# Performance work log

Measured on AMD Instinct MI355X. Metric: run time of the kernel, lower is better.

## Reference

```python
import jax, jax.numpy as jnp
import numpy as np

N_NODES = 50000
N_GRAPHS = 128


def gcn_conv(x, W, b, src, dst, n_nodes):
    """PyG-style GCNConv: add self-loops, symmetric normalization, linear transform, scatter-add."""
    # linear transform first (PyG applies lin before propagate)
    h = x @ W  # [N, out]
    loop = jnp.arange(n_nodes, dtype=src.dtype)
    src_f = jnp.concatenate([src, loop])  # [E+N]
    dst_f = jnp.concatenate([dst, loop])
    # degree over destination (incl. self-loops), edge weight = 1
    deg = jax.ops.segment_sum(jnp.ones_like(src_f, dtype=h.dtype), dst_f, num_segments=n_nodes)
    dinv = jnp.where(deg > 0, jax.lax.rsqrt(deg), 0.0)
    norm = dinv[src_f] * dinv[dst_f]  # [E+N]
    msg = h[src_f] * norm[:, None]  # gather + scale
    out = jax.ops.segment_sum(msg, dst_f, num_segments=n_nodes)  # scatter-add
    return out + b


def setup_inputs() -> dict:
    key = jax.random.key(0)
    k = jax.random.split(key, 8)
    in_c, hid_c, out_c = 128, 128, 64
    x = jax.random.normal(k[0], (N_NODES, in_c), dtype=jnp.float32)
    edge_index = jax.random.randint(k[1], (2, 625000), 0, N_NODES, dtype=jnp.int64)
    batch = jnp.sort(jax.random.randint(k[2], (N_NODES,), 0, N_GRAPHS, dtype=jnp.int64))
    # Glorot-style init for GCN weights, zero bias (PyG default)
    W1 = jax.random.normal(k[3], (in_c, hid_c), dtype=jnp.float32) / np.sqrt(in_c)
    b1 = jnp.zeros((hid_c,), dtype=jnp.float32)
    W2 = jax.random.normal(k[4], (hid_c, out_c), dtype=jnp.float32) / np.sqrt(hid_c)
    b2 = jnp.zeros((out_c,), dtype=jnp.float32)
    return {"x": x, "W1": W1, "b1": b1, "W2": W2, "b2": b2,
            "edge_index": edge_index, "batch": batch}


def reference(x, W1, b1, W2, b2, edge_index, batch):
    src, dst = edge_index[0], edge_index[1]
    h = gcn_conv(x, W1, b1, src, dst, N_NODES)
    h = jax.nn.relu(h)
    h = gcn_conv(h, W2, b2, src, dst, N_NODES)  # [N, out_c]
    # global_mean_pool: segment mean over batch vector
    sums = jax.ops.segment_sum(h, batch, num_segments=N_GRAPHS)  # [G, out_c]
    counts = jax.ops.segment_sum(jnp.ones((h.shape[0],), dtype=h.dtype), batch, num_segments=N_GRAPHS)
    return sums / jnp.maximum(counts, 1.0)[:, None]
```

## Files before the change

kernel.cpp:

```cpp
#include <hip/hip_runtime.h>
#include <hip/hip_bf16.h>
#include <hip/hip_fp8.h>
#include <stdint.h>

typedef __hip_bfloat16  bf16;
typedef __hip_bfloat162 bf2;

typedef __attribute__((ext_vector_type(8))) short short8v;
typedef __attribute__((ext_vector_type(4))) float float4v;

#define KSLOT 48
#define CSTRIDE 16

static __device__ __forceinline__ uint32_t pack2(float a, float b) {
  bf2 t = __float22bfloat162_rn(make_float2(a, b));
  return *(uint32_t*)&t;
}
static __device__ __forceinline__ float fp8_to_f(unsigned char b) {
  __hip_fp8_e4m3 t; t.__x = (__hip_fp8_storage_t)b; return (float)t;
}
static __device__ __forceinline__ unsigned char f_to_fp8(float f) {
  __hip_fp8_e4m3 t(f); return (unsigned char)t.__x;
}

union U16x8 { uint32_t u[4]; uint4 q; short8v v; };

#define NB_FILL 306
#define NB_GEMM 782


__global__ void k_prep(const float* __restrict__ W1, const float* __restrict__ W2,
                       ushort* __restrict__ Ws1, ushort* __restrict__ Ws2,
                       const int* __restrict__ batch, int* __restrict__ gstart,
                       int n, int G) {
  const int tid = threadIdx.x;
  if (blockIdx.x == 0) {
    for (int idx = tid; idx < 2048; idx += 256) {
      int t = idx >> 8, c = (idx >> 6) & 3, l = idx & 63;
      int kbase = c * 32 + (l >> 4) * 8, colg = t * 16 + (l & 15);
      U16x8 u;
#pragma unroll
      for (int j = 0; j < 4; ++j)
        u.u[j] = pack2(W1[(size_t)(kbase + 2 * j) * 128 + colg],
                       W1[(size_t)(kbase + 2 * j + 1) * 128 + colg]);
      *(uint4*)&Ws1[(size_t)idx * 8] = u.q;
    }
  } else {
    for (int idx = tid; idx < 1024; idx += 256) {
      int t = idx >> 8, c = (idx >> 6) & 3, l = idx & 63;
      int kbase = c * 32 + (l >> 4) * 8, colg = t * 16 + (l & 15);
      U16x8 u;
#pragma unroll
      for (int j = 0; j < 4; ++j)
        u.u[j] = pack2(W2[(size_t)(kbase + 2 * j) * 64 + colg],
                       W2[(size_t)(kbase + 2 * j + 1) * 64 + colg]);
      *(uint4*)&Ws2[(size_t)idx * 8] = u.q;
    }
    if (tid <= G) {
      int lo = 0, hi = n;
      while (lo < hi) {
        int mid = (lo + hi) >> 1;
        if (batch[mid] < tid) lo = mid + 1; else hi = mid;
      }
      gstart[tid] = lo;
    }
  }
}


__global__ __launch_bounds__(256) void k_fused(
    const float* __restrict__ A, const ushort* __restrict__ Ws1,
    unsigned char* __restrict__ C, int n,
    const int* __restrict__ src, const int* __restrict__ dst,
    int* __restrict__ cntS, ushort* __restrict__ slots, int E) {
  __shared__ ushort Wf[2048 * 8];
  const int bid = blockIdx.x;
  const int tid = threadIdx.x;

  if (bid < NB_FILL) {
    int base = bid * 2048 + tid;
#pragma unroll
    for (int j = 0; j < 8; ++j) {
      int e = base + j * 256;
      if (e < E) {
        int d = dst[e];
        int p = atomicAdd(&cntS[d << 4], 1);
        if (p < KSLOT) slots[(size_t)d * KSLOT + p] = (ushort)src[e];
      }
    }
  } else {
    for (int idx = tid; idx < 2048; idx += 256)
      *(uint4*)&Wf[(size_t)idx * 8] = *(const uint4*)&Ws1[(size_t)idx * 8];
    __syncthreads();
    const int row0 = (bid - NB_FILL) * 64;
    const int w = tid >> 6, lane = tid & 63;
    const int m = lane & 15, q = lane >> 4;
    const int gr = row0 + w * 16 + m;
    float4v acc[8];
#pragma unroll
    for (int t = 0; t < 8; ++t) acc[t] = (float4v){0.f, 0.f, 0.f, 0.f};
    for (int c = 0; c < 4; ++c) {
      U16x8 a;
      if (gr < n) {
        const float* ap = &A[(size_t)gr * 128 + c * 32 + q * 8];
        float4 f0 = *(const float4*)ap;
        float4 f1 = *(const float4*)(ap + 4);
        a.u[0] = pack2(f0.x, f0.y); a.u[1] = pack2(f0.z, f0.w);
        a.u[2] = pack2(f1.x, f1.y); a.u[3] = pack2(f1.z, f1.w);
      } else {
        a.q = make_uint4(0, 0, 0, 0);
      }
#pragma unroll
      for (int t = 0; t < 8; ++t) {
        U16x8 b;
        b.q = *(const uint4*)&Wf[((size_t)(t * 4 + c) * 64 + lane) * 8];
        acc[t] = __builtin_amdgcn_mfma_f32_16x16x32_bf16(a.v, b.v, acc[t], 0, 0, 0);
      }
    }
#pragma unroll
    for (int reg = 0; reg < 4; ++reg) {
      int gor = row0 + w * 16 + q * 4 + reg;
      if (gor < n) {
#pragma unroll
        for (int t = 0; t < 8; ++t)
          C[(size_t)gor * 128 + t * 16 + m] = f_to_fp8(acc[t][reg]);
      }
    }
  }
}

__global__ void k_dinv(const int* __restrict__ cntS, float* __restrict__ dinv, int n) {
  int i = blockIdx.x * blockDim.x + threadIdx.x;
  if (i < n) dinv[i] = rsqrtf((float)(cntS[i << 4] + 1));
}


__global__ __launch_bounds__(256) void k_gemm64(const bf16* __restrict__ A,
                                                const ushort* __restrict__ Ws2,
                                                unsigned char* __restrict__ C, int n) {
  __shared__ ushort Wf[1024 * 8];
  const int tid = threadIdx.x;
  const int row0 = blockIdx.x * 64;
  for (int idx = tid; idx < 1024; idx += 256)
    *(uint4*)&Wf[(size_t)idx * 8] = *(const uint4*)&Ws2[(size_t)idx * 8];
  __syncthreads();
  const int w = tid >> 6, lane = tid & 63;
  const int m = lane & 15, q = lane >> 4;
  const int gr = row0 + w * 16 + m;
  float4v acc[4];
#pragma unroll
  for (int t = 0; t < 4; ++t) acc[t] = (float4v){0.f, 0.f, 0.f, 0.f};
  for (int c = 0; c < 4; ++c) {
    U16x8 a;
    if (gr < n) {
      a.q = *(const uint4*)&A[(size_t)gr * 128 + c * 32 + q * 8];
    } else {
      a.q = make_uint4(0, 0, 0, 0);
    }
#pragma unroll
    for (int t = 0; t < 4; ++t) {
      U16x8 b;
      b.q = *(const uint4*)&Wf[((size_t)(t * 4 + c) * 64 + lane) * 8];
      acc[t] = __builtin_amdgcn_mfma_f32_16x16x32_bf16(a.v, b.v, acc[t], 0, 0, 0);
    }
  }
#pragma unroll
  for (int reg = 0; reg < 4; ++reg) {
    int gor = row0 + w * 16 + q * 4 + reg;
    if (gor < n) {
#pragma unroll
      for (int t = 0; t < 4; ++t)
        C[(size_t)gor * 64 + t * 16 + m] = f_to_fp8(acc[t][reg]);
    }
  }
}


__global__ void k_agg1(const unsigned char* __restrict__ h, const float* __restrict__ dinv,
                       const int* __restrict__ cntS, const ushort* __restrict__ slots,
                       const float* __restrict__ b1, bf16* __restrict__ out, int n) {
  int wid = threadIdx.x >> 6, lane = threadIdx.x & 63;
  int v = blockIdx.x * 4 + wid;
  if (v >= n) return;
  float dv = dinv[v];
  ushort sraw = ((const ushort*)(h + (size_t)v * 128))[lane];
  float ax = fp8_to_f((unsigned char)(sraw & 0xff)) * dv;
  float ay = fp8_to_f((unsigned char)(sraw >> 8)) * dv;
  int deg = min(cntS[v << 4], KSLOT);
  const ushort* sl = slots + (size_t)v * KSLOT;
  for (int e = 0; e < deg; e += 8) {
    uint4 u8 = *(const uint4*)&sl[e];
    int id[8] = {(int)(u8.x & 0xffff), (int)(u8.x >> 16), (int)(u8.y & 0xffff), (int)(u8.y >> 16),
                 (int)(u8.z & 0xffff), (int)(u8.z >> 16), (int)(u8.w & 0xffff), (int)(u8.w >> 16)};
    float w[8];
#pragma unroll
    for (int j = 0; j < 8; ++j) {
      bool live = (e + j < deg);
      id[j] = live ? id[j] : v;
      w[j] = live ? dinv[id[j]] : 0.f;
    }
    ushort raw[8];
#pragma unroll
    for (int j = 0; j < 8; ++j)
      raw[j] = ((const ushort*)(h + (size_t)id[j] * 128))[lane];
#pragma unroll
    for (int j = 0; j < 8; ++j) {
      ax += w[j] * fp8_to_f((unsigned char)(raw[j] & 0xff));
      ay += w[j] * fp8_to_f((unsigned char)(raw[j] >> 8));
    }
  }
  float2 bb = ((const float2*)b1)[lane];
  float rx = fmaxf(ax * dv + bb.x, 0.f);
  float ry = fmaxf(ay * dv + bb.y, 0.f);
  ((bf2*)(out + (size_t)v * 128))[lane] = __float22bfloat162_rn(make_float2(rx, ry));
}

__global__ void k_agg2(const unsigned char* __restrict__ h, const float* __restrict__ dinv,
                       const int* __restrict__ cntS, const ushort* __restrict__ slots,
                       const float* __restrict__ b2, float* __restrict__ o2, int n) {
  int wid = threadIdx.x >> 6, lane = threadIdx.x & 63;
  int v = blockIdx.x * 4 + wid;
  if (v >= n) return;
  float dv = dinv[v];
  float acc = fp8_to_f(h[(size_t)v * 64 + lane]) * dv;
  int deg = min(cntS[v << 4], KSLOT);
  const ushort* sl = slots + (size_t)v * KSLOT;
  for (int e = 0; e < deg; e += 8) {
    uint4 u8 = *(const uint4*)&sl[e];
    int id[8] = {(int)(u8.x & 0xffff), (int)(u8.x >> 16), (int)(u8.y & 0xffff), (int)(u8.y >> 16),
                 (int)(u8.z & 0xffff), (int)(u8.z >> 16), (int)(u8.w & 0xffff), (int)(u8.w >> 16)};
    float w[8];
#pragma unroll
    for (int j = 0; j < 8; ++j) {
      bool live = (e + j < deg);
      id[j] = live ? id[j] : v;
      w[j] = live ? dinv[id[j]] : 0.f;
    }
    unsigned char raw[8];
#pragma unroll
    for (int j = 0; j < 8; ++j)
      raw[j] = h[(size_t)id[j] * 64 + lane];
#pragma unroll
    for (int j = 0; j < 8; ++j) acc += w[j] * fp8_to_f(raw[j]);
  }
  o2[(size_t)v * 64 + lane] = acc * dv + b2[lane];
}

__global__ void k_pool(const float* __restrict__ o2, const int* __restrict__ gstart,
                       float* __restrict__ out) {
  int g = blockIdx.x;
  int s = gstart[g], epos = gstart[g + 1];
  int lane = threadIdx.x & 63, wid = threadIdx.x >> 6;
  float acc = 0.f;
  for (int i = s + wid; i < epos; i += 4)
    acc += o2[(size_t)i * 64 + lane];
  __shared__ float red[4][64];
  red[wid][lane] = acc;
  __syncthreads();
  if (wid == 0) {
    float v = red[0][lane] + red[1][lane] + red[2][lane] + red[3][lane];
    float c = (float)max(epos - s, 1);
    out[g * 64 + lane] = v / c;
  }
}


extern "C" void kernel_launch(void* const* d_in, const int* in_sizes, int n_in,
                              void* d_out, int out_size, void* d_ws, size_t ws_size,
                              hipStream_t stream) {
  const float* x   = (const float*)d_in[0];
  const float* W1  = (const float*)d_in[1];
  const float* b1  = (const float*)d_in[2];
  const float* W2  = (const float*)d_in[3];
  const float* b2  = (const float*)d_in[4];
  const int* ei    = (const int*)d_in[5];
  const int* batch = (const int*)d_in[6];

  const int n = in_sizes[0] / 128;
  const int E = in_sizes[5] / 2;
  const int G = 128;

  const int* src = ei;
  const int* dst = ei + E;

  char* ws = (char*)d_ws;
  size_t off = 0;
  auto alloc = [&](size_t bytes) -> void* {
    void* p = ws + off;
    off = (off + bytes + 255) & ~(size_t)255;
    return p;
  };
  unsigned char* h1 = (unsigned char*)alloc((size_t)n * 128);
  bf16*   a1    = (bf16*)alloc((size_t)n * 128 * 2);
  ushort* slots = (ushort*)alloc((size_t)n * KSLOT * 2);
  int*    cntS  = (int*)alloc((size_t)n * CSTRIDE * 4);
  float*  dinv  = (float*)alloc((size_t)n * 4);
  int*    gstart= (int*)alloc((size_t)(G + 1) * 4);
  ushort* Ws1   = (ushort*)alloc(2048 * 16);
  ushort* Ws2   = (ushort*)alloc(1024 * 16);
  unsigned char* h2 = h1;
  float*  o2 = (float*)a1;
  float*  out = (float*)d_out;

  hipMemsetAsync(cntS, 0, (size_t)n * CSTRIDE * 4, stream);

  k_prep<<<2, 256, 0, stream>>>(W1, W2, Ws1, Ws2, batch, gstart, n, G);
  k_fused<<<NB_FILL + NB_GEMM, 256, 0, stream>>>(x, Ws1, h1, n, src, dst, cntS, slots, E);
  k_dinv<<<(n + 255) / 256, 256, 0, stream>>>(cntS, dinv, n);
  k_agg1<<<(n + 3) / 4, 256, 0, stream>>>(h1, dinv, cntS, slots, b1, a1, n);
  k_gemm64<<<(n + 63) / 64, 256, 0, stream>>>(a1, Ws2, h2, n);
  k_agg2<<<(n + 3) / 4, 256, 0, stream>>>(h2, dinv, cntS, slots, b2, o2, n);
  k_pool<<<G, 256, 0, stream>>>(o2, gstart, out);
}
```

Before: 206.4 us.

## Fuse layer-1 aggregation with second GEMM and pooling into aggregation via atomics

Merges the layer-1 aggregation, ReLU and the 128x64 MFMA GEMM into one kernel that keeps each 16-node tile of activations in shared memory, so the bf16 intermediate never goes to global memory. It also folds mean pooling into the layer-2 aggregation through atomicAdd scaled by a precomputed inverse graph size, with the output pre-seeded with the bias. Finally, the cntS memset moves into extra blocks of the prep kernel. This removes two kernel launches, a memset and intermediate global traffic. In exchange it adds atomic contention on the 128x64 output and gives lower occupancy in the fused kernel. The cntS zeroing hardcodes 200000 uint4 chunks, which assumes n equals 50000.

```diff
diff --git a/kernel.cpp b/kernel.cpp
--- a/kernel.cpp
+++ b/kernel.cpp
@@ -27,14 +27,17 @@
 
 #define NB_FILL 306
 #define NB_GEMM 782
+#define NZB 196
 
 
 __global__ void k_prep(const float* __restrict__ W1, const float* __restrict__ W2,
                        ushort* __restrict__ Ws1, ushort* __restrict__ Ws2,
                        const int* __restrict__ batch, int* __restrict__ gstart,
-                       int n, int G) {
+                       float* __restrict__ inv_ng, const float* __restrict__ b2,
+                       float* __restrict__ out, int* __restrict__ cntS, int n, int G) {
   const int tid = threadIdx.x;
-  if (blockIdx.x == 0) {
+  const int bid = blockIdx.x;
+  if (bid == 0) {
     for (int idx = tid; idx < 2048; idx += 256) {
       int t = idx >> 8, c = (idx >> 6) & 3, l = idx & 63;
       int kbase = c * 32 + (l >> 4) * 8, colg = t * 16 + (l & 15);
@@ -45,7 +48,8 @@
                        W1[(size_t)(kbase + 2 * j + 1) * 128 + colg]);
       *(uint4*)&Ws1[(size_t)idx * 8] = u.q;
     }
-  } else {
+  } else if (bid == 1) {
+    __shared__ int gs[129];
     for (int idx = tid; idx < 1024; idx += 256) {
       int t = idx >> 8, c = (idx >> 6) & 3, l = idx & 63;
       int kbase = c * 32 + (l >> 4) * 8, colg = t * 16 + (l & 15);
@@ -63,6 +67,16 @@
         if (batch[mid] < tid) lo = mid + 1; else hi = mid;
       }
       gstart[tid] = lo;
+      gs[tid] = lo;
+    }
+    __syncthreads();
+    if (tid < G) inv_ng[tid] = 1.f / (float)max(gs[tid + 1] - gs[tid], 1);
+    for (int i = tid; i < G * 64; i += 256) out[i] = b2[i & 63];
+  } else {
+    int b = bid - 2;
+    for (int i = tid; i < 1024; i += 256) {
+      int idx4 = b * 1024 + i;
+      if (idx4 < 200000) *(uint4*)&cntS[idx4 * 4] = make_uint4(0, 0, 0, 0);
     }
   }
 }
@@ -135,89 +149,80 @@
 }
 
 
-__global__ __launch_bounds__(256) void k_gemm64(const bf16* __restrict__ A,
-                                                const ushort* __restrict__ Ws2,
-                                                unsigned char* __restrict__ C, int n) {
+#define A1STR 136
+__global__ __launch_bounds__(256) void k_ag1g2(
+    const unsigned char* __restrict__ h, const float* __restrict__ dinv,
+    const int* __restrict__ cntS, const ushort* __restrict__ slots,
+    const float* __restrict__ b1, const ushort* __restrict__ Ws2,
+    unsigned char* __restrict__ H2, int n) {
   __shared__ ushort Wf[1024 * 8];
+  __shared__ ushort a1s[16 * A1STR];
   const int tid = threadIdx.x;
-  const int row0 = blockIdx.x * 64;
+  const int wid = tid >> 6, lane = tid & 63;
+  const int base = blockIdx.x * 16;
+
   for (int idx = tid; idx < 1024; idx += 256)
     *(uint4*)&Wf[(size_t)idx * 8] = *(const uint4*)&Ws2[(size_t)idx * 8];
+
+  float2 bb = ((const float2*)b1)[lane];
+  for (int s = 0; s < 4; ++s) {
+    int nl = wid * 4 + s;
+    int v = base + nl;
+    if (v < n) {
+      float dv = dinv[v];
+      ushort sraw = ((const ushort*)(h + (size_t)v * 128))[lane];
+      float ax = fp8_to_f((unsigned char)(sraw & 0xff)) * dv;
+      float ay = fp8_to_f((unsigned char)(sraw >> 8)) * dv;
+      int deg = min(cntS[v << 4], KSLOT);
+      const ushort* sl = slots + (size_t)v * KSLOT;
+      for (int e = 0; e < deg; e += 8) {
+        uint4 u8 = *(const uint4*)&sl[e];
+        int id[8] = {(int)(u8.x & 0xffff), (int)(u8.x >> 16), (int)(u8.y & 0xffff), (int)(u8.y >> 16),
+                     (int)(u8.z & 0xffff), (int)(u8.z >> 16), (int)(u8.w & 0xffff), (int)(u8.w >> 16)};
+        float w[8];
+#pragma unroll
+        for (int j = 0; j < 8; ++j) {
+          bool live = (e + j < deg);
+          id[j] = live ? id[j] : v;
+          w[j] = live ? dinv[id[j]] : 0.f;
+        }
+        ushort raw[8];
+#pragma unroll
+        for (int j = 0; j < 8; ++j)
+          raw[j] = ((const ushort*)(h + (size_t)id[j] * 128))[lane];
+#pragma unroll
+        for (int j = 0; j < 8; ++j) {
+          ax += w[j] * fp8_to_f((unsigned char)(raw[j] & 0xff));
+          ay += w[j] * fp8_to_f((unsigned char)(raw[j] >> 8));
+        }
+      }
+      float rx = fmaxf(ax * dv + bb.x, 0.f);
+      float ry = fmaxf(ay * dv + bb.y, 0.f);
+      *(uint32_t*)&a1s[nl * A1STR + lane * 2] = pack2(rx, ry);
+    }
+  }
   __syncthreads();
-  const int w = tid >> 6, lane = tid & 63;
+
   const int m = lane & 15, q = lane >> 4;
-  const int gr = row0 + w * 16 + m;
-  float4v acc[4];
-#pragma unroll
-  for (int t = 0; t < 4; ++t) acc[t] = (float4v){0.f, 0.f, 0.f, 0.f};
+  float4v acc = (float4v){0.f, 0.f, 0.f, 0.f};
   for (int c = 0; c < 4; ++c) {
-    U16x8 a;
-    if (gr < n) {
-      a.q = *(const uint4*)&A[(size_t)gr * 128 + c * 32 + q * 8];
-    } else {
-      a.q = make_uint4(0, 0, 0, 0);
-    }
-#pragma unroll
-    for (int t = 0; t < 4; ++t) {
-      U16x8 b;
-      b.q = *(const uint4*)&Wf[((size_t)(t * 4 + c) * 64 + lane) * 8];
-      acc[t] = __builtin_amdgcn_mfma_f32_16x16x32_bf16(a.v, b.v, acc[t], 0, 0, 0);
-    }
+    U16x8 a, b;
+    a.q = *(const uint4*)&a1s[m * A1STR + c * 32 + q * 8];
+    b.q = *(const uint4*)&Wf[((size_t)(wid * 4 + c) * 64 + lane) * 8];
+    acc = __builtin_amdgcn_mfma_f32_16x16x32_bf16(a.v, b.v, acc, 0, 0, 0);
   }
 #pragma unroll
   for (int reg = 0; reg < 4; ++reg) {
-    int gor = row0 + w * 16 + q * 4 + reg;
-    if (gor < n) {
-#pragma unroll
-      for (int t = 0; t < 4; ++t)
-        C[(size_t)gor * 64 + t * 16 + m] = f_to_fp8(acc[t][reg]);
-    }
-  }
-}
-
-
-__global__ void k_agg1(const unsigned char* __restrict__ h, const float* __restrict__ dinv,
+    int gor = base + q * 4 + reg;
+    if (gor < n) H2[(size_t)gor * 64 + wid * 16 + m] = f_to_fp8(acc[reg]);
+  }
+}
+
+
+__global__ void k_ag2p(const unsigned char* __restrict__ h, const float* __restrict__ dinv,
                        const int* __restrict__ cntS, const ushort* __restrict__ slots,
-                       const float* __restrict__ b1, bf16* __restrict__ out, int n) {
-  int wid = threadIdx.x >> 6, lane = threadIdx.x & 63;
-  int v = blockIdx.x * 4 + wid;
-  if (v >= n) return;
-  float dv = dinv[v];
-  ushort sraw = ((const ushort*)(h + (size_t)v * 128))[lane];
-  float ax = fp8_to_f((unsigned char)(sraw & 0xff)) * dv;
-  float ay = fp8_to_f((unsigned char)(sraw >> 8)) * dv;
-  int deg = min(cntS[v << 4], KSLOT);
-  const ushort* sl = slots + (size_t)v * KSLOT;
-  for (int e = 0; e < deg; e += 8) {
-    uint4 u8 = *(const uint4*)&sl[e];
-    int id[8] = {(int)(u8.x & 0xffff), (int)(u8.x >> 16), (int)(u8.y & 0xffff), (int)(u8.y >> 16),
-                 (int)(u8.z & 0xffff), (int)(u8.z >> 16), (int)(u8.w & 0xffff), (int)(u8.w >> 16)};
-    float w[8];
-#pragma unroll
-    for (int j = 0; j < 8; ++j) {
-      bool live = (e + j < deg);
-      id[j] = live ? id[j] : v;
-      w[j] = live ? dinv[id[j]] : 0.f;
-    }
-    ushort raw[8];
-#pragma unroll
-    for (int j = 0; j < 8; ++j)
-      raw[j] = ((const ushort*)(h + (size_t)id[j] * 128))[lane];
-#pragma unroll
-    for (int j = 0; j < 8; ++j) {
-      ax += w[j] * fp8_to_f((unsigned char)(raw[j] & 0xff));
-      ay += w[j] * fp8_to_f((unsigned char)(raw[j] >> 8));
-    }
-  }
-  float2 bb = ((const float2*)b1)[lane];
-  float rx = fmaxf(ax * dv + bb.x, 0.f);
-  float ry = fmaxf(ay * dv + bb.y, 0.f);
-  ((bf2*)(out + (size_t)v * 128))[lane] = __float22bfloat162_rn(make_float2(rx, ry));
-}
-
-__global__ void k_agg2(const unsigned char* __restrict__ h, const float* __restrict__ dinv,
-                       const int* __restrict__ cntS, const ushort* __restrict__ slots,
-                       const float* __restrict__ b2, float* __restrict__ o2, int n) {
+                       const int* __restrict__ batch, const float* __restrict__ inv_ng,
+                       float* __restrict__ out, int n) {
   int wid = threadIdx.x >> 6, lane = threadIdx.x & 63;
   int v = blockIdx.x * 4 + wid;
   if (v >= n) return;
@@ -243,25 +248,8 @@
 #pragma unroll
     for (int j = 0; j < 8; ++j) acc += w[j] * fp8_to_f(raw[j]);
   }
-  o2[(size_t)v * 64 + lane] = acc * dv + b2[lane];
-}
-
-__global__ void k_pool(const float* __restrict__ o2, const int* __restrict__ gstart,
-                       float* __restrict__ out) {
-  int g = blockIdx.x;
-  int s = gstart[g], epos = gstart[g + 1];
-  int lane = threadIdx.x & 63, wid = threadIdx.x >> 6;
-  float acc = 0.f;
-  for (int i = s + wid; i < epos; i += 4)
-    acc += o2[(size_t)i * 64 + lane];
-  __shared__ float red[4][64];
-  red[wid][lane] = acc;
-  __syncthreads();
-  if (wid == 0) {
-    float v = red[0][lane] + red[1][lane] + red[2][lane] + red[3][lane];
-    float c = (float)max(epos - s, 1);
-    out[g * 64 + lane] = v / c;
-  }
+  int g = batch[v];
+  atomicAdd(&out[(size_t)g * 64 + lane], acc * dv * inv_ng[g]);
 }
 
 
@@ -291,24 +279,20 @@
     return p;
   };
   unsigned char* h1 = (unsigned char*)alloc((size_t)n * 128);
-  bf16*   a1    = (bf16*)alloc((size_t)n * 128 * 2);
+  unsigned char* H2 = (unsigned char*)alloc((size_t)n * 64);
   ushort* slots = (ushort*)alloc((size_t)n * KSLOT * 2);
   int*    cntS  = (int*)alloc((size_t)n * CSTRIDE * 4);
   float*  dinv  = (float*)alloc((size_t)n * 4);
   int*    gstart= (int*)alloc((size_t)(G + 1) * 4);
+  float*  invng = (float*)alloc((size_t)G * 4);
   ushort* Ws1   = (ushort*)alloc(2048 * 16);
   ushort* Ws2   = (ushort*)alloc(1024 * 16);
-  unsigned char* h2 = h1;
-  float*  o2 = (float*)a1;
   float*  out = (float*)d_out;
 
-  hipMemsetAsync(cntS, 0, (size_t)n * CSTRIDE * 4, stream);
-
-  k_prep<<<2, 256, 0, stream>>>(W1, W2, Ws1, Ws2, batch, gstart, n, G);
+  k_prep<<<2 + NZB, 256, 0, stream>>>(W1, W2, Ws1, Ws2, batch, gstart, invng, b2,
+                                      out, cntS, n, G);
   k_fused<<<NB_FILL + NB_GEMM, 256, 0, stream>>>(x, Ws1, h1, n, src, dst, cntS, slots, E);
   k_dinv<<<(n + 255) / 256, 256, 0, stream>>>(cntS, dinv, n);
-  k_agg1<<<(n + 3) / 4, 256, 0, stream>>>(h1, dinv, cntS, slots, b1, a1, n);
-  k_gemm64<<<(n + 63) / 64, 256, 0, stream>>>(a1, Ws2, h2, n);
-  k_agg2<<<(n + 3) / 4, 256, 0, stream>>>(h2, dinv, cntS, slots, b2, o2, n);
-  k_pool<<<G, 256, 0, stream>>>(o2, gstart, out);
-}
+  k_ag1g2<<<(n + 15) / 16, 256, 0, stream>>>(h1, dinv, cntS, slots, b1, Ws2, H2, n);
+  k_ag2p<<<(n + 3) / 4, 256, 0, stream>>>(H2, dinv, cntS, slots, batch, invng, out, n);
+}
```

After: 202.3 us. No clear change (-2.0%).
